# Optimization experiments

Measured on AMD Instinct MI355X. Metric: run time of the kernel, lower is better.

The kernel has to match this reference:

```python
import jax, jax.numpy as jnp
import numpy as np

NUM_EVENT_TYPES = 100000
EMBED_DIM = 16
SEQ_LEN = 4194304
TAU = 0.1


def setup_inputs() -> dict:
    key = jax.random.key(0)
    k1, k2, k3, k4, k5 = jax.random.split(key, 5)
    event_trace = jax.random.randint(k1, (SEQ_LEN,), 0, NUM_EVENT_TYPES, dtype=jnp.int32)
    embed_table = jax.random.normal(k2, (NUM_EVENT_TYPES, EMBED_DIM), dtype=jnp.float32)
    w_attn = jax.random.normal(k3, (EMBED_DIM,), dtype=jnp.float32) * (1.0 / np.sqrt(EMBED_DIM))
    b_attn = jax.random.normal(k4, (), dtype=jnp.float32) * 0.01
    causality_logits = jnp.zeros((NUM_EVENT_TYPES,), dtype=jnp.float32)
    return {
        "event_trace": event_trace,
        "is_crash": 1,
        "embed_table": embed_table,
        "w_attn": w_attn,
        "b_attn": b_attn,
        "causality_logits": causality_logits,
    }


def reference(event_trace, is_crash, embed_table, w_attn, b_attn, causality_logits):
    # gather embeddings: [S, D]
    embeds = embed_table[event_trace]
    # attn projection to scalar logit per position: [S]
    attn_logits = embeds @ w_attn + b_attn
    # softmax over the whole trace
    attn_weights = jax.nn.softmax(attn_logits / TAU, axis=0)
    # scatter-add attention mass per event type (segment sum): [T]
    type_attention = jax.ops.segment_sum(attn_weights, event_trace,
                                         num_segments=NUM_EVENT_TYPES)
    # type_attention is zero for types absent from the trace, so summing over
    # all types equals the original's sum over unique(event_trace).
    causality = jax.nn.sigmoid(causality_logits)
    explained = jnp.clip(jnp.sum(type_attention * causality), 0.0, 1.0)
    contradiction = jnp.where(jnp.asarray(is_crash) > 0.5,
                              jax.nn.relu(1.0 - explained),
                              jax.nn.relu(explained))
    return contradiction
```

## Files before the change

kernel.cpp:

```cpp
#include <hip/hip_runtime.h>
#include <math.h>

namespace {

constexpr float kInvTau = 10.0f;
constexpr float kShift  = 50.0f;
constexpr int   kBlock      = 256;
constexpr int   kPBlock     = 1024;
constexpr int   kElemPT     = 16;
constexpr int   kChunkTypes = 36864;
constexpr int   kNChunk     = 3;
constexpr int   kTPad       = kChunkTypes * kNChunk;
constexpr int   kVPT        = kChunkTypes / 4 / kPBlock;

typedef int      v4i __attribute__((ext_vector_type(4)));
typedef unsigned v4u __attribute__((ext_vector_type(4)));

__device__ __forceinline__ unsigned bf16bits(float x) {
    unsigned u = __float_as_uint(x);
    unsigned r = u + 0x7fffu + ((u >> 16) & 1u);
    return r & 0xffff0000u;
}
__device__ __forceinline__ float hi16f(unsigned q) { return __uint_as_float(q & 0xffff0000u); }
__device__ __forceinline__ float lo16f(unsigned q) { return __uint_as_float(q << 16); }

__global__ __launch_bounds__(kBlock)
void prep_kernel(const float* __restrict__ table,
                 const float* __restrict__ w,
                 const float* __restrict__ b,
                 const float* __restrict__ cl,
                 unsigned* __restrict__ g4,
                 unsigned* __restrict__ ticket, int T) {
    int t = blockIdx.x * blockDim.x + threadIdx.x;
    if (t == 0) *ticket = 0u;
    if (t >= kTPad) return;
    if (t >= T) { g4[t] = 0u; return; }
    const float4* row = reinterpret_cast<const float4*>(table) + (size_t)t * 4;
    const float4* wv  = reinterpret_cast<const float4*>(w);
    float4 r0 = row[0], r1 = row[1], r2 = row[2], r3 = row[3];
    float4 w0 = wv[0],  w1 = wv[1],  w2 = wv[2],  w3 = wv[3];
    float dot = r0.x*w0.x + r0.y*w0.y + r0.z*w0.z + r0.w*w0.w
              + r1.x*w1.x + r1.y*w1.y + r1.z*w1.z + r1.w*w1.w
              + r2.x*w2.x + r2.y*w2.y + r2.z*w2.z + r2.w*w2.w
              + r3.x*w3.x + r3.y*w3.y + r3.z*w3.z + r3.w*w3.w;
    float p = (dot + b[0]) * kInvTau - kShift;
    float e = __expf(p);
    float c = 1.0f / (1.0f + __expf(-cl[t]));
    g4[t] = bf16bits(e) | (bf16bits(e * c) >> 16);
}

__global__ __launch_bounds__(kPBlock)
void pass_kernel(const int* __restrict__ trace, int S,
                 const unsigned* __restrict__ g4,
                 float2* __restrict__ blk,
                 unsigned* __restrict__ ticket,
                 const int* __restrict__ is_crash,
                 float* __restrict__ out) {
    __shared__ unsigned lds[kChunkTypes];
    __shared__ float    wsum[16], wtum[16];
    __shared__ int      last;

    const int tid = threadIdx.x;

    const v4i* trace4 = reinterpret_cast<const v4i*>(trace);
    const int  base4  = blockIdx.x * (kPBlock * kElemPT / 4);
    v4i ia = __builtin_nontemporal_load(&trace4[base4 + 0 * kPBlock + tid]);
    v4i ib = __builtin_nontemporal_load(&trace4[base4 + 1 * kPBlock + tid]);
    v4i ic = __builtin_nontemporal_load(&trace4[base4 + 2 * kPBlock + tid]);
    v4i id = __builtin_nontemporal_load(&trace4[base4 + 3 * kPBlock + tid]);

    v4u r[kVPT];
    {
        const v4u* src = reinterpret_cast<const v4u*>(g4);
        #pragma unroll
        for (int j = 0; j < kVPT; ++j) r[j] = src[j * kPBlock + tid];
        v4u* dst = reinterpret_cast<v4u*>(lds);
        #pragma unroll
        for (int j = 0; j < kVPT; ++j) dst[j * kPBlock + tid] = r[j];
    }
    __syncthreads();

    float s = 0.f, t = 0.f;
    #pragma unroll
    for (int c = 0; c < kNChunk; ++c) {
        if (c + 1 < kNChunk) {
            const v4u* src = reinterpret_cast<const v4u*>(g4 + (c + 1) * kChunkTypes);
            #pragma unroll
            for (int j = 0; j < kVPT; ++j) r[j] = src[j * kPBlock + tid];
        }
        const int base = c * kChunkTypes;
        #define ACC(IDX) do {                                    \
            int      _o = (IDX) - base;                          \
            bool     _v = (unsigned)_o < (unsigned)kChunkTypes;  \
            unsigned _q = lds[_v ? _o : (tid & 63)];             \
            _q = _v ? _q : 0u;                                   \
            s += hi16f(_q);                                      \
            t += lo16f(_q);                                      \
        } while (0)
        ACC(ia.x); ACC(ia.y); ACC(ia.z); ACC(ia.w);
        ACC(ib.x); ACC(ib.y); ACC(ib.z); ACC(ib.w);
        ACC(ic.x); ACC(ic.y); ACC(ic.z); ACC(ic.w);
        ACC(id.x); ACC(id.y); ACC(id.z); ACC(id.w);
        #undef ACC
        __syncthreads();
        if (c + 1 < kNChunk) {
            v4u* dst = reinterpret_cast<v4u*>(lds);
            #pragma unroll
            for (int j = 0; j < kVPT; ++j) dst[j * kPBlock + tid] = r[j];
            __syncthreads();
        }
    }

    const int covered = (int)(gridDim.x) * kPBlock * kElemPT;
    for (int i = covered + blockIdx.x * kPBlock + tid; i < S;
         i += gridDim.x * kPBlock) {
        unsigned q = g4[trace[i]];
        s += hi16f(q); t += lo16f(q);
    }

    #pragma unroll
    for (int off = 1; off < 64; off <<= 1) {
        s += __shfl_xor(s, off);
        t += __shfl_xor(t, off);
    }
    const int lane = tid & 63, wave = tid >> 6;
    if (lane == 0) { wsum[wave] = s; wtum[wave] = t; }
    __syncthreads();
    if (tid == 0) {
        #pragma unroll
        for (int i = 1; i < kPBlock / 64; ++i) { s += wsum[i]; t += wtum[i]; }
        __hip_atomic_store(&blk[blockIdx.x].x, s, __ATOMIC_RELAXED, __HIP_MEMORY_SCOPE_AGENT);
        __hip_atomic_store(&blk[blockIdx.x].y, t, __ATOMIC_RELAXED, __HIP_MEMORY_SCOPE_AGENT);
        __threadfence();
        unsigned rr = atomicAdd(ticket, 1u);
        last = (rr == (unsigned)(gridDim.x - 1)) ? 1 : 0;
    }
    __syncthreads();
    if (!last) return;

    __threadfence();
    float s2 = 0.f, t2 = 0.f;
    for (int i = tid; i < (int)gridDim.x; i += kPBlock) {
        s2 += __hip_atomic_load(&blk[i].x, __ATOMIC_RELAXED, __HIP_MEMORY_SCOPE_AGENT);
        t2 += __hip_atomic_load(&blk[i].y, __ATOMIC_RELAXED, __HIP_MEMORY_SCOPE_AGENT);
    }
    #pragma unroll
    for (int off = 1; off < 64; off <<= 1) {
        s2 += __shfl_xor(s2, off);
        t2 += __shfl_xor(t2, off);
    }
    if (lane == 0) { wsum[wave] = s2; wtum[wave] = t2; }
    __syncthreads();
    if (tid == 0) {
        #pragma unroll
        for (int i = 1; i < kPBlock / 64; ++i) { s2 += wsum[i]; t2 += wtum[i]; }
        float explained = (s2 > 0.f) ? (t2 / s2) : 0.f;
        explained = fminf(fmaxf(explained, 0.f), 1.f);
        out[0] = (is_crash[0] > 0) ? fmaxf(1.0f - explained, 0.f)
                                   : fmaxf(explained, 0.f);
    }
}

}

extern "C" void kernel_launch(void* const* d_in, const int* in_sizes, int n_in,
                              void* d_out, int out_size, void* d_ws, size_t ws_size,
                              hipStream_t stream) {
    const int*   trace = (const int*)  d_in[0];
    const int*   crash = (const int*)  d_in[1];
    const float* table = (const float*)d_in[2];
    const float* w     = (const float*)d_in[3];
    const float* b     = (const float*)d_in[4];
    const float* cl    = (const float*)d_in[5];
    float*       out   = (float*)d_out;

    const int S = in_sizes[0];
    const int T = in_sizes[5];

    char* p = (char*)d_ws;
    unsigned* g4  = (unsigned*)p;  p += (size_t)kTPad * sizeof(unsigned);
    float2*   blk = (float2*)p;

    int gridP = S / (kPBlock * kElemPT);
    if (gridP < 1) gridP = 1;
    unsigned* ticket = (unsigned*)(p + (size_t)gridP * sizeof(float2));

    int gridT = (kTPad + kBlock - 1) / kBlock;
    prep_kernel<<<gridT, kBlock, 0, stream>>>(table, w, b, cl, g4, ticket, T);
    pass_kernel<<<gridP, kPBlock, 0, stream>>>(trace, S, g4, blk, ticket, crash, out);
}
```

Baseline: 28.28 us.

## Split packed table into bf16 exp and 8-bit causality, two LDS chunks

Replaces the 32-bit packed per-type value (bf16 e and bf16 e*c) with a 16-bit bf16 exp array plus an 8-bit quantized sigmoid array. This shrinks the per-type table from 4 to 3 bytes, so the type range fits in two LDS chunks instead of three, removing one full table reload and one barrier pair per block. Odd blocks load the chunks in reverse order, and the second chunk is prefetched into registers alongside the trace load. The cost is 8-bit quantization of causality, which lowers accuracy, plus an extra multiply and byte LDS read per element.

```diff
diff --git a/kernel.cpp b/kernel.cpp
--- a/kernel.cpp
+++ b/kernel.cpp
@@ -5,36 +5,36 @@
 
 constexpr float kInvTau = 10.0f;
 constexpr float kShift  = 50.0f;
-constexpr int   kBlock      = 256;
-constexpr int   kPBlock     = 1024;
-constexpr int   kElemPT     = 16;
-constexpr int   kChunkTypes = 36864;
-constexpr int   kNChunk     = 3;
-constexpr int   kTPad       = kChunkTypes * kNChunk;
-constexpr int   kVPT        = kChunkTypes / 4 / kPBlock;
+constexpr int   kBlock   = 256;
+constexpr int   kPBlock  = 1024;
+constexpr int   kElemPT  = 16;
+constexpr int   kChunkT  = 53248;
+constexpr int   kNChunk  = 2;
+constexpr int   kTPad    = kChunkT * kNChunk;
+constexpr int   kEV      = kChunkT / 2 / kPBlock;
+constexpr int   kCV      = kChunkT / 4 / kPBlock;
 
 typedef int      v4i __attribute__((ext_vector_type(4)));
-typedef unsigned v4u __attribute__((ext_vector_type(4)));
+typedef unsigned v2u __attribute__((ext_vector_type(2)));
 
 __device__ __forceinline__ unsigned bf16bits(float x) {
     unsigned u = __float_as_uint(x);
     unsigned r = u + 0x7fffu + ((u >> 16) & 1u);
     return r & 0xffff0000u;
 }
-__device__ __forceinline__ float hi16f(unsigned q) { return __uint_as_float(q & 0xffff0000u); }
-__device__ __forceinline__ float lo16f(unsigned q) { return __uint_as_float(q << 16); }
 
 __global__ __launch_bounds__(kBlock)
 void prep_kernel(const float* __restrict__ table,
                  const float* __restrict__ w,
                  const float* __restrict__ b,
                  const float* __restrict__ cl,
-                 unsigned* __restrict__ g4,
+                 unsigned short* __restrict__ e16g,
+                 unsigned char*  __restrict__ c8g,
                  unsigned* __restrict__ ticket, int T) {
     int t = blockIdx.x * blockDim.x + threadIdx.x;
     if (t == 0) *ticket = 0u;
     if (t >= kTPad) return;
-    if (t >= T) { g4[t] = 0u; return; }
+    if (t >= T) { e16g[t] = 0; c8g[t] = 0; return; }
     const float4* row = reinterpret_cast<const float4*>(table) + (size_t)t * 4;
     const float4* wv  = reinterpret_cast<const float4*>(w);
     float4 r0 = row[0], r1 = row[1], r2 = row[2], r3 = row[3];
@@ -46,21 +46,35 @@
     float p = (dot + b[0]) * kInvTau - kShift;
     float e = __expf(p);
     float c = 1.0f / (1.0f + __expf(-cl[t]));
-    g4[t] = bf16bits(e) | (bf16bits(e * c) >> 16);
+    e16g[t] = (unsigned short)(bf16bits(e) >> 16);
+    c8g[t]  = (unsigned char)fminf(255.0f, rintf(c * 256.0f));
 }
 
 __global__ __launch_bounds__(kPBlock)
 void pass_kernel(const int* __restrict__ trace, int S,
-                 const unsigned* __restrict__ g4,
+                 const unsigned short* __restrict__ e16g,
+                 const unsigned char*  __restrict__ c8g,
                  float2* __restrict__ blk,
                  unsigned* __restrict__ ticket,
                  const int* __restrict__ is_crash,
                  float* __restrict__ out) {
-    __shared__ unsigned lds[kChunkTypes];
-    __shared__ float    wsum[16], wtum[16];
-    __shared__ int      last;
+    __shared__ unsigned short eLds[kChunkT];
+    __shared__ unsigned char  cLds[kChunkT];
+    __shared__ float wsum[16], wtum[16];
+    __shared__ int   last;
 
     const int tid = threadIdx.x;
+    const int k0  = blockIdx.x & 1;
+    const int B0  = k0 ? kChunkT : 0;
+    const int B1  = k0 ? 0 : kChunkT;
+
+    const v2u*      esrc0 = reinterpret_cast<const v2u*>(e16g + B0);
+    const unsigned* csrc0 = reinterpret_cast<const unsigned*>(c8g + B0);
+    v2u re0[kEV]; unsigned rc0[kCV];
+    #pragma unroll
+    for (int j = 0; j < kEV; ++j) re0[j] = esrc0[j * kPBlock + tid];
+    #pragma unroll
+    for (int j = 0; j < kCV; ++j) rc0[j] = csrc0[j * kPBlock + tid];
 
     const v4i* trace4 = reinterpret_cast<const v4i*>(trace);
     const int  base4  = blockIdx.x * (kPBlock * kElemPT / 4);
@@ -69,53 +83,63 @@
     v4i ic = __builtin_nontemporal_load(&trace4[base4 + 2 * kPBlock + tid]);
     v4i id = __builtin_nontemporal_load(&trace4[base4 + 3 * kPBlock + tid]);
 
-    v4u r[kVPT];
+    const v2u*      esrc1 = reinterpret_cast<const v2u*>(e16g + B1);
+    const unsigned* csrc1 = reinterpret_cast<const unsigned*>(c8g + B1);
+    v2u re1[kEV]; unsigned rc1[kCV];
+    #pragma unroll
+    for (int j = 0; j < kEV; ++j) re1[j] = esrc1[j * kPBlock + tid];
+    #pragma unroll
+    for (int j = 0; j < kCV; ++j) rc1[j] = csrc1[j * kPBlock + tid];
+
     {
-        const v4u* src = reinterpret_cast<const v4u*>(g4);
-        #pragma unroll
-        for (int j = 0; j < kVPT; ++j) r[j] = src[j * kPBlock + tid];
-        v4u* dst = reinterpret_cast<v4u*>(lds);
-        #pragma unroll
-        for (int j = 0; j < kVPT; ++j) dst[j * kPBlock + tid] = r[j];
+        v2u*      edst = reinterpret_cast<v2u*>(eLds);
+        unsigned* cdst = reinterpret_cast<unsigned*>(cLds);
+        #pragma unroll
+        for (int j = 0; j < kEV; ++j) edst[j * kPBlock + tid] = re0[j];
+        #pragma unroll
+        for (int j = 0; j < kCV; ++j) cdst[j * kPBlock + tid] = rc0[j];
     }
     __syncthreads();
 
     float s = 0.f, t = 0.f;
-    #pragma unroll
-    for (int c = 0; c < kNChunk; ++c) {
-        if (c + 1 < kNChunk) {
-            const v4u* src = reinterpret_cast<const v4u*>(g4 + (c + 1) * kChunkTypes);
-            #pragma unroll
-            for (int j = 0; j < kVPT; ++j) r[j] = src[j * kPBlock + tid];
-        }
-        const int base = c * kChunkTypes;
-        #define ACC(IDX) do {                                    \
-            int      _o = (IDX) - base;                          \
-            bool     _v = (unsigned)_o < (unsigned)kChunkTypes;  \
-            unsigned _q = lds[_v ? _o : (tid & 63)];             \
-            _q = _v ? _q : 0u;                                   \
-            s += hi16f(_q);                                      \
-            t += lo16f(_q);                                      \
-        } while (0)
-        ACC(ia.x); ACC(ia.y); ACC(ia.z); ACC(ia.w);
-        ACC(ib.x); ACC(ib.y); ACC(ib.z); ACC(ib.w);
-        ACC(ic.x); ACC(ic.y); ACC(ic.z); ACC(ic.w);
-        ACC(id.x); ACC(id.y); ACC(id.z); ACC(id.w);
-        #undef ACC
-        __syncthreads();
-        if (c + 1 < kNChunk) {
-            v4u* dst = reinterpret_cast<v4u*>(lds);
-            #pragma unroll
-            for (int j = 0; j < kVPT; ++j) dst[j * kPBlock + tid] = r[j];
-            __syncthreads();
-        }
-    }
+    #define ACC(IDX, BASE) do {                                   \
+        int      _o = (IDX) - (BASE);                             \
+        bool     _v = (unsigned)_o < (unsigned)kChunkT;           \
+        int      _a = _v ? _o : (tid & 63);                       \
+        unsigned _eb = eLds[_a];                                  \
+        float    _e  = _v ? __uint_as_float(_eb << 16) : 0.f;     \
+        float    _cf = (float)cLds[_a];                           \
+        s += _e;  t += _e * _cf;                                  \
+    } while (0)
+
+    ACC(ia.x, B0); ACC(ia.y, B0); ACC(ia.z, B0); ACC(ia.w, B0);
+    ACC(ib.x, B0); ACC(ib.y, B0); ACC(ib.z, B0); ACC(ib.w, B0);
+    ACC(ic.x, B0); ACC(ic.y, B0); ACC(ic.z, B0); ACC(ic.w, B0);
+    ACC(id.x, B0); ACC(id.y, B0); ACC(id.z, B0); ACC(id.w, B0);
+    __syncthreads();
+
+    {
+        v2u*      edst = reinterpret_cast<v2u*>(eLds);
+        unsigned* cdst = reinterpret_cast<unsigned*>(cLds);
+        #pragma unroll
+        for (int j = 0; j < kEV; ++j) edst[j * kPBlock + tid] = re1[j];
+        #pragma unroll
+        for (int j = 0; j < kCV; ++j) cdst[j * kPBlock + tid] = rc1[j];
+    }
+    __syncthreads();
+
+    ACC(ia.x, B1); ACC(ia.y, B1); ACC(ia.z, B1); ACC(ia.w, B1);
+    ACC(ib.x, B1); ACC(ib.y, B1); ACC(ib.z, B1); ACC(ib.w, B1);
+    ACC(ic.x, B1); ACC(ic.y, B1); ACC(ic.z, B1); ACC(ic.w, B1);
+    ACC(id.x, B1); ACC(id.y, B1); ACC(id.z, B1); ACC(id.w, B1);
+    #undef ACC
 
     const int covered = (int)(gridDim.x) * kPBlock * kElemPT;
     for (int i = covered + blockIdx.x * kPBlock + tid; i < S;
          i += gridDim.x * kPBlock) {
-        unsigned q = g4[trace[i]];
-        s += hi16f(q); t += lo16f(q);
+        int idx = trace[i];
+        float e = __uint_as_float((unsigned)e16g[idx] << 16);
+        s += e;  t += e * (float)c8g[idx];
     }
 
     #pragma unroll
@@ -154,7 +178,7 @@
     if (tid == 0) {
         #pragma unroll
         for (int i = 1; i < kPBlock / 64; ++i) { s2 += wsum[i]; t2 += wtum[i]; }
-        float explained = (s2 > 0.f) ? (t2 / s2) : 0.f;
+        float explained = (s2 > 0.f) ? (t2 / (256.0f * s2)) : 0.f;
         explained = fminf(fmaxf(explained, 0.f), 1.f);
         out[0] = (is_crash[0] > 0) ? fmaxf(1.0f - explained, 0.f)
                                    : fmaxf(explained, 0.f);
@@ -178,14 +202,15 @@
     const int T = in_sizes[5];
 
     char* p = (char*)d_ws;
-    unsigned* g4  = (unsigned*)p;  p += (size_t)kTPad * sizeof(unsigned);
-    float2*   blk = (float2*)p;
+    unsigned short* e16g = (unsigned short*)p;  p += (size_t)kTPad * sizeof(unsigned short);
+    unsigned char*  c8g  = (unsigned char*)p;   p += (size_t)kTPad * sizeof(unsigned char);
+    float2*         blk  = (float2*)p;
 
     int gridP = S / (kPBlock * kElemPT);
     if (gridP < 1) gridP = 1;
     unsigned* ticket = (unsigned*)(p + (size_t)gridP * sizeof(float2));
 
     int gridT = (kTPad + kBlock - 1) / kBlock;
-    prep_kernel<<<gridT, kBlock, 0, stream>>>(table, w, b, cl, g4, ticket, T);
-    pass_kernel<<<gridP, kPBlock, 0, stream>>>(trace, S, g4, blk, ticket, crash, out);
-}
+    prep_kernel<<<gridT, kBlock, 0, stream>>>(table, w, b, cl, e16g, c8g, ticket, T);
+    pass_kernel<<<gridP, kPBlock, 0, stream>>>(trace, S, e16g, c8g, blk, ticket, crash, out);
+}
```

New measurement: 37.60 us. +33.0%, slower.
